# Kernel tuning notes

Hardware: AMD Instinct MI355X
Metric: run time of the kernel (lower is better)

## Reference

```python
import jax, jax.numpy as jnp
import numpy as np

TAIL_BOUND = 3.0
MIN_BIN_WIDTH = 1e-3
MIN_BIN_HEIGHT = 1e-3
SEARCH_EPS = 1e-6


def setup_inputs() -> dict:
    key = jax.random.key(0)
    k1, k2, k3, k4, k5 = jax.random.split(key, 5)
    B, D, K = 8192, 256, 8
    return {
        "x": jax.random.normal(k1, (B, D), dtype=jnp.float32),
        "w_": jax.random.normal(k2, (B, D, K), dtype=jnp.float32),
        "h_": jax.random.normal(k3, (B, D, K), dtype=jnp.float32),
        "dl_": jax.random.normal(k4, (B, D, 1), dtype=jnp.float32),
        "dr_": jax.random.normal(k5, (B, D, 1), dtype=jnp.float32),
    }


def _cumknots(unnorm, min_bin):
    # softmax -> min-width floor -> cumsum with exact 0/1 endpoints
    num_bins = unnorm.shape[-1]
    w = jax.nn.softmax(unnorm, axis=-1)
    w = min_bin + (1.0 - min_bin * num_bins) * w
    cum = jnp.cumsum(w, axis=-1)
    cum = cum.at[..., -1].set(1.0)
    pad = [(0, 0)] * (cum.ndim - 1) + [(1, 0)]
    cum = jnp.pad(cum, pad)
    return w, cum


def reference(x, w_, h_, dl_, dr_):
    num_bins = w_.shape[-1]
    left = bottom = -TAIL_BOUND
    right = top = TAIL_BOUND

    inside = (x >= left) & (x <= right)

    # map to unit interval; clamp keeps masked-out lanes numerically safe
    t = jnp.clip((x - left) / (right - left), 0.0, 1.0)

    widths, cumwidths = _cumknots(w_, MIN_BIN_WIDTH)       # [B,D,K], [B,D,K+1]
    heights, cumheights = _cumknots(h_, MIN_BIN_HEIGHT)

    slopes = heights / widths                              # [B,D,K]
    min1 = jnp.minimum(jnp.abs(slopes[..., :-1]), jnp.abs(slopes[..., 1:]))
    min2 = 0.5 * (widths[..., 1:] * slopes[..., :-1] + widths[..., :-1] * slopes[..., 1:]) \
           / (widths[..., :-1] + widths[..., 1:])
    mins = jnp.minimum(min1, min2)                         # [B,D,K-1]

    d_left = jax.nn.sigmoid(dl_) * 3.0 * slopes[..., :1]
    d_right = jax.nn.sigmoid(dr_) * 3.0 * slopes[..., -1:]
    d_mid = mins * (jnp.sign(slopes[..., :-1]) + jnp.sign(slopes[..., 1:]))
    derivs = jnp.concatenate([d_left, d_mid, d_right], axis=-1)  # [B,D,K+1]

    a = (derivs[..., :-1] + derivs[..., 1:] - 2.0 * slopes) / widths ** 2
    b = (3.0 * slopes - 2.0 * derivs[..., :-1] - derivs[..., 1:]) / widths
    c = derivs[..., :-1]
    d = cumheights[..., :-1]

    # searchsorted: sum(t >= knots) - 1, with eps bump on the last knot
    knots = cumwidths.at[..., -1].add(SEARCH_EPS)
    bin_idx = jnp.sum((t[..., None] >= knots).astype(jnp.int32), axis=-1) - 1
    bin_idx = jnp.clip(bin_idx, 0, num_bins - 1)[..., None]  # [B,D,1]

    take = lambda arr: jnp.take_along_axis(arr, bin_idx, axis=-1)[..., 0]
    ia, ib, ic, id_ = take(a), take(b), take(c), take(d)
    lw = take(cumwidths)

    sx = t - lw
    out_s = ia * sx ** 3 + ib * sx ** 2 + ic * sx + id_
    lad_s = jnp.log(jnp.abs(3.0 * ia * sx ** 2 + 2.0 * ib * sx + ic))

    out_s = jnp.clip(out_s, 0.0, 1.0) * (top - bottom) + bottom
    lad_s = lad_s + jnp.log(top - bottom) - jnp.log(right - left)

    outputs = jnp.where(inside, out_s, x)          # identity tails
    logabsdet = jnp.where(inside, lad_s, 0.0)
    return outputs, logabsdet
```

## Files before the change

### kernel.cpp

```cpp
#include <hip/hip_runtime.h>
#include <math.h>


constexpr int K = 8;
constexpr float TAIL = 3.0f;
constexpr float MIN_BIN = 0.001f;

__device__ __forceinline__ float rcpf(float v) {
    return __builtin_amdgcn_rcpf(v);
}

__device__ __forceinline__ unsigned swz(unsigned off) {
    return off ^ ((off >> 3) & 0x70u);
}

__global__ __launch_bounds__(256) void cbs_kernel(
    const float* __restrict__ x_,
    const float* __restrict__ w_,
    const float* __restrict__ h_,
    const float* __restrict__ dl_,
    const float* __restrict__ dr_,
    float* __restrict__ out,
    float* __restrict__ lad,
    int n)
{
    __shared__ __align__(16) unsigned char lds[16384];

    int i = blockIdx.x * blockDim.x + threadIdx.x;
    if (i >= n) return;

    int wave = threadIdx.x >> 6;
    int lane = threadIdx.x & 63;
    size_t ebase = (size_t)blockIdx.x * 256 + (size_t)wave * 64;

    const char* wg = (const char*)w_ + ebase * 32;
    const char* hg = (const char*)h_ + ebase * 32;
    unsigned wb = (unsigned)wave * 4096u;
    unsigned hb = wb + 2048u;

    #pragma unroll
    for (int r = 0; r < 2; r++) {
        unsigned off = (unsigned)(r * 1024 + 16 * lane);
        float4 vw = *(const float4*)(wg + off);
        float4 vh = *(const float4*)(hg + off);
        *(float4*)(&lds[wb + swz(off)]) = vw;
        *(float4*)(&lds[hb + swz(off)]) = vh;
    }

    float xv  = x_[i];
    float dlv = dl_[i];
    float drv = dr_[i];

    unsigned o0 = 32u * (unsigned)lane;
    float4 wa  = *(const float4*)(&lds[wb + swz(o0)]);
    float4 wbv = *(const float4*)(&lds[wb + swz(o0 + 16u)]);
    float4 ha  = *(const float4*)(&lds[hb + swz(o0)]);
    float4 hbv = *(const float4*)(&lds[hb + swz(o0 + 16u)]);

    float wr[K] = {wa.x, wa.y, wa.z, wa.w, wbv.x, wbv.y, wbv.z, wbv.w};
    float hr[K] = {ha.x, ha.y, ha.z, ha.w, hbv.x, hbv.y, hbv.z, hbv.w};

    float sw = 0.0f, sh = 0.0f;
    #pragma unroll
    for (int k = 0; k < K; k++) { wr[k] = __expf(wr[k]); sw += wr[k]; }
    #pragma unroll
    for (int k = 0; k < K; k++) { hr[k] = __expf(hr[k]); sh += hr[k]; }
    float cwf = (1.0f - MIN_BIN * K) * rcpf(sw);
    float chf = (1.0f - MIN_BIN * K) * rcpf(sh);
    #pragma unroll
    for (int k = 0; k < K; k++) {
        wr[k] = fmaf(wr[k], cwf, MIN_BIN);
        hr[k] = fmaf(hr[k], chf, MIN_BIN);
    }

    float cw[K + 1], ch[K + 1], s[K];
    cw[0] = 0.0f; ch[0] = 0.0f;
    #pragma unroll
    for (int k = 0; k < K; k++) {
        cw[k + 1] = cw[k] + wr[k];
        ch[k + 1] = ch[k] + hr[k];
        s[k] = hr[k] * rcpf(wr[k]);
    }

    float dv[K + 1];
    dv[0] = 3.0f * s[0]     * rcpf(1.0f + __expf(-dlv));
    dv[K] = 3.0f * s[K - 1] * rcpf(1.0f + __expf(-drv));
    #pragma unroll
    for (int k = 0; k < K - 1; k++) {
        float num = wr[k + 1] * s[k] + wr[k] * s[k + 1];
        dv[k + 1] = fminf(2.0f * fminf(s[k], s[k + 1]),
                          num * rcpf(wr[k] + wr[k + 1]));
    }

    float t = fminf(fmaxf((xv + TAIL) * (1.0f / (2.0f * TAIL)), 0.0f), 1.0f);

    float wk = wr[0], sk = s[0], d0 = dv[0], d1 = dv[1], lw = 0.0f, dd = 0.0f;
    #pragma unroll
    for (int k = 1; k < K; k++) {
        bool p = (t >= cw[k]);
        wk = p ? wr[k]     : wk;
        sk = p ? s[k]      : sk;
        d0 = p ? dv[k]     : d0;
        d1 = p ? dv[k + 1] : d1;
        lw = p ? cw[k]     : lw;
        dd = p ? ch[k]     : dd;
    }

    float iw = rcpf(wk);
    float ia = (d0 + d1 - 2.0f * sk) * iw * iw;
    float ib = (3.0f * sk - 2.0f * d0 - d1) * iw;
    float sx = t - lw;
    float out_s = ((ia * sx + ib) * sx + d0) * sx + dd;
    float der   = (3.0f * ia * sx + 2.0f * ib) * sx + d0;
    float lad_s = __logf(fabsf(der));

    out_s = fminf(fmaxf(out_s, 0.0f), 1.0f) * (2.0f * TAIL) - TAIL;

    bool inside = (xv >= -TAIL) && (xv <= TAIL);
    out[i] = inside ? out_s : xv;
    lad[i] = inside ? lad_s : 0.0f;
}

extern "C" void kernel_launch(void* const* d_in, const int* in_sizes, int n_in,
                              void* d_out, int out_size, void* d_ws, size_t ws_size,
                              hipStream_t stream) {
    const float* x  = (const float*)d_in[0];
    const float* w  = (const float*)d_in[1];
    const float* h  = (const float*)d_in[2];
    const float* dl = (const float*)d_in[3];
    const float* dr = (const float*)d_in[4];
    int n = in_sizes[0];
    float* out = (float*)d_out;
    float* lad = out + n;

    const int threads = 256;
    const int blocks = (n + threads - 1) / threads;
    cbs_kernel<<<blocks, threads, 0, stream>>>(x, w, h, dl, dr, out, lad, n);
}
```

Baseline: 175.6 us.

## Process multiple elements per thread with software-pipelined register prefetch

New measurement: 176.8 us. No clear change (+0.7%).

```diff
diff --git a/kernel.cpp b/kernel.cpp
--- a/kernel.cpp
+++ b/kernel.cpp
@@ -3,6 +3,7 @@
 
 
 constexpr int K = 8;
+constexpr int ITERS = 8;
 constexpr float TAIL = 3.0f;
 constexpr float MIN_BIN = 0.001f;
 
@@ -10,55 +11,34 @@
     return __builtin_amdgcn_rcpf(v);
 }
 
-__device__ __forceinline__ unsigned swz(unsigned off) {
-    return off ^ ((off >> 3) & 0x70u);
+struct Elem {
+    float4 wa, wb, ha, hb;
+    float x, dl, dr;
+};
+
+__device__ __forceinline__ Elem load_elem(
+    const float* __restrict__ x_, const float* __restrict__ w_,
+    const float* __restrict__ h_, const float* __restrict__ dl_,
+    const float* __restrict__ dr_, int i)
+{
+    Elem e;
+    const float4* w4 = (const float4*)w_ + 2 * (size_t)i;
+    const float4* h4 = (const float4*)h_ + 2 * (size_t)i;
+    e.wa = w4[0]; e.wb = w4[1];
+    e.ha = h4[0]; e.hb = h4[1];
+    e.x  = x_[i];
+    e.dl = dl_[i];
+    e.dr = dr_[i];
+    return e;
 }
 
-__global__ __launch_bounds__(256) void cbs_kernel(
-    const float* __restrict__ x_,
-    const float* __restrict__ w_,
-    const float* __restrict__ h_,
-    const float* __restrict__ dl_,
-    const float* __restrict__ dr_,
-    float* __restrict__ out,
-    float* __restrict__ lad,
-    int n)
+__device__ __forceinline__ void process(
+    const Elem& el, float* __restrict__ out, float* __restrict__ lad, int i)
 {
-    __shared__ __align__(16) unsigned char lds[16384];
-
-    int i = blockIdx.x * blockDim.x + threadIdx.x;
-    if (i >= n) return;
-
-    int wave = threadIdx.x >> 6;
-    int lane = threadIdx.x & 63;
-    size_t ebase = (size_t)blockIdx.x * 256 + (size_t)wave * 64;
-
-    const char* wg = (const char*)w_ + ebase * 32;
-    const char* hg = (const char*)h_ + ebase * 32;
-    unsigned wb = (unsigned)wave * 4096u;
-    unsigned hb = wb + 2048u;
-
-    #pragma unroll
-    for (int r = 0; r < 2; r++) {
-        unsigned off = (unsigned)(r * 1024 + 16 * lane);
-        float4 vw = *(const float4*)(wg + off);
-        float4 vh = *(const float4*)(hg + off);
-        *(float4*)(&lds[wb + swz(off)]) = vw;
-        *(float4*)(&lds[hb + swz(off)]) = vh;
-    }
-
-    float xv  = x_[i];
-    float dlv = dl_[i];
-    float drv = dr_[i];
-
-    unsigned o0 = 32u * (unsigned)lane;
-    float4 wa  = *(const float4*)(&lds[wb + swz(o0)]);
-    float4 wbv = *(const float4*)(&lds[wb + swz(o0 + 16u)]);
-    float4 ha  = *(const float4*)(&lds[hb + swz(o0)]);
-    float4 hbv = *(const float4*)(&lds[hb + swz(o0 + 16u)]);
-
-    float wr[K] = {wa.x, wa.y, wa.z, wa.w, wbv.x, wbv.y, wbv.z, wbv.w};
-    float hr[K] = {ha.x, ha.y, ha.z, ha.w, hbv.x, hbv.y, hbv.z, hbv.w};
+    float wr[K] = {el.wa.x, el.wa.y, el.wa.z, el.wa.w,
+                   el.wb.x, el.wb.y, el.wb.z, el.wb.w};
+    float hr[K] = {el.ha.x, el.ha.y, el.ha.z, el.ha.w,
+                   el.hb.x, el.hb.y, el.hb.z, el.hb.w};
 
     float sw = 0.0f, sh = 0.0f;
     #pragma unroll
@@ -83,8 +63,8 @@
     }
 
     float dv[K + 1];
-    dv[0] = 3.0f * s[0]     * rcpf(1.0f + __expf(-dlv));
-    dv[K] = 3.0f * s[K - 1] * rcpf(1.0f + __expf(-drv));
+    dv[0] = 3.0f * s[0]     * rcpf(1.0f + __expf(-el.dl));
+    dv[K] = 3.0f * s[K - 1] * rcpf(1.0f + __expf(-el.dr));
     #pragma unroll
     for (int k = 0; k < K - 1; k++) {
         float num = wr[k + 1] * s[k] + wr[k] * s[k + 1];
@@ -92,7 +72,7 @@
                           num * rcpf(wr[k] + wr[k + 1]));
     }
 
-    float t = fminf(fmaxf((xv + TAIL) * (1.0f / (2.0f * TAIL)), 0.0f), 1.0f);
+    float t = fminf(fmaxf((el.x + TAIL) * (1.0f / (2.0f * TAIL)), 0.0f), 1.0f);
 
     float wk = wr[0], sk = s[0], d0 = dv[0], d1 = dv[1], lw = 0.0f, dd = 0.0f;
     #pragma unroll
@@ -116,9 +96,41 @@
 
     out_s = fminf(fmaxf(out_s, 0.0f), 1.0f) * (2.0f * TAIL) - TAIL;
 
-    bool inside = (xv >= -TAIL) && (xv <= TAIL);
-    out[i] = inside ? out_s : xv;
+    bool inside = (el.x >= -TAIL) && (el.x <= TAIL);
+    out[i] = inside ? out_s : el.x;
     lad[i] = inside ? lad_s : 0.0f;
+}
+
+__global__ __launch_bounds__(256) void cbs_kernel(
+    const float* __restrict__ x_,
+    const float* __restrict__ w_,
+    const float* __restrict__ h_,
+    const float* __restrict__ dl_,
+    const float* __restrict__ dr_,
+    float* __restrict__ out,
+    float* __restrict__ lad,
+    int n)
+{
+    int stride = gridDim.x * blockDim.x;
+    int i = blockIdx.x * blockDim.x + threadIdx.x;
+
+    if (i >= n) return;
+    Elem cur = load_elem(x_, w_, h_, dl_, dr_, i);
+
+    #pragma unroll
+    for (int it = 0; it < ITERS; ++it) {
+        int inext = i + stride;
+        Elem nxt;
+        bool have_next = (it + 1 < ITERS) && (inext < n);
+        if (have_next)
+            nxt = load_elem(x_, w_, h_, dl_, dr_, inext);
+
+        process(cur, out, lad, i);
+
+        cur = nxt;
+        i = inext;
+        if (!have_next) break;
+    }
 }
 
 extern "C" void kernel_launch(void* const* d_in, const int* in_sizes, int n_in,
@@ -134,6 +146,7 @@
     float* lad = out + n;
 
     const int threads = 256;
-    const int blocks = (n + threads - 1) / threads;
+    const int per_block = threads * ITERS;
+    const int blocks = (n + per_block - 1) / per_block;
     cbs_kernel<<<blocks, threads, 0, stream>>>(x, w, h, dl, dr, out, lad, n);
 }
```
